# Performance work log

Measured on AMD Instinct MI355X. Metric: run time of the kernel, lower is better.

The kernel has to match this reference:

```python
import jax, jax.numpy as jnp
import numpy as np

N_HEAD = 16
N_EMBED = 2048


def setup_inputs() -> dict:
    key = jax.random.key(0)
    k1, k2, k3, k4, k5 = jax.random.split(key, 5)
    B, T, C = 4, 2048, N_EMBED
    scale = 1.0 / np.sqrt(C)
    return {
        "x": jax.random.normal(k1, (B, T, C), dtype=jnp.float32),
        "w_attn": jax.random.normal(k2, (C, 3 * C), dtype=jnp.float32) * scale,
        "b_attn": jnp.zeros((3 * C,), dtype=jnp.float32),
        "w_proj": jax.random.normal(k3, (C, C), dtype=jnp.float32) * scale,
        "b_proj": jnp.zeros((C,), dtype=jnp.float32),
    }


def reference(x, w_attn, b_attn, w_proj, b_proj):
    B, T, C = x.shape
    H = N_HEAD
    hd = C // H
    # fused QKV projection: [B,T,3C]
    qkv = jnp.einsum("btc,cd->btd", x, w_attn) + b_attn
    q, k, v = jnp.split(qkv, 3, axis=-1)
    # [B,H,T,hd]
    q = q.reshape(B, T, H, hd).transpose(0, 2, 1, 3)
    k = k.reshape(B, T, H, hd).transpose(0, 2, 1, 3)
    v = v.reshape(B, T, H, hd).transpose(0, 2, 1, 3)
    # scaled dot-product attention (no mask, no dropout at eval)
    scores = jnp.einsum("bhqd,bhkd->bhqk", q, k) / jnp.sqrt(jnp.asarray(hd, dtype=q.dtype))
    attn = jax.nn.softmax(scores, axis=-1)
    y = jnp.einsum("bhqk,bhkd->bhqd", attn, v)
    y = y.transpose(0, 2, 1, 3).reshape(B, T, C)
    return jnp.einsum("btc,cd->btd", y, w_proj) + b_proj
```

## Files before the change

kernel.cpp:

```cpp
#include <hip/hip_runtime.h>
#include <hip/hip_fp16.h>

typedef _Float16 f16;
typedef _Float16 half8 __attribute__((ext_vector_type(8)));
typedef float f32x4 __attribute__((ext_vector_type(4)));

#define NBAT 4
#define NT   2048
#define NC   2048
#define NHEAD 16
#define HD   128
#define NM   8192
#define N3C  6144
#define QK_LD 4096
#define ATT_SCALE 0.088388347648318447f

static __device__ __forceinline__ void gload16(const void* g, void* l) {
  __builtin_amdgcn_global_load_lds(
      (const __attribute__((address_space(1))) unsigned int*)g,
      (__attribute__((address_space(3))) unsigned int*)l, 16, 0, 0);
}


__global__ __launch_bounds__(256) void cvt_x_f16(const float* __restrict__ in,
                                                 f16* __restrict__ out) {
  size_t i = ((size_t)blockIdx.x * 256 + threadIdx.x) * 8;
  float4 a = *(const float4*)(in + i);
  float4 b = *(const float4*)(in + i + 4);
  half8 o;
  o[0] = (f16)a.x; o[1] = (f16)a.y; o[2] = (f16)a.z; o[3] = (f16)a.w;
  o[4] = (f16)b.x; o[5] = (f16)b.y; o[6] = (f16)b.z; o[7] = (f16)b.w;
  *(half8*)(out + i) = o;
}

__global__ __launch_bounds__(256) void cvt_tr_f16(const float* __restrict__ in,
                                                  f16* __restrict__ out,
                                                  int R, int CC) {
  __shared__ float tile[32][33];
  int cb = blockIdx.x * 32, rb = blockIdx.y * 32;
  int lx = threadIdx.x & 31, ly = threadIdx.x >> 5;
  for (int i = 0; i < 32; i += 8)
    tile[ly + i][lx] = in[(size_t)(rb + ly + i) * CC + cb + lx];
  __syncthreads();
  for (int i = 0; i < 32; i += 8)
    out[(size_t)(cb + ly + i) * R + rb + lx] = (f16)tile[lx][ly + i];
}

template <int OUTMODE>
__global__ __launch_bounds__(512, 2)
void gemm256(const f16* __restrict__ A, const f16* __restrict__ BT,
             const float* __restrict__ bias,
             f16* __restrict__ oqk, f16* __restrict__ ovT,
             float* __restrict__ of32, int N, int K, int nbn) {
  __shared__ f16 sA[4 * 8192];
  __shared__ f16 sB[4 * 8192];

  const int tid = threadIdx.x;
  const int wv = tid >> 6, lane = tid & 63;
  const int lr = lane & 15, lg = lane >> 4;
  const int wm = wv >> 2, wn = wv & 3;

  const int bid = blockIdx.x;
  const int xcd = bid & 7, li = bid >> 3;
  const int nbh = nbn >> 1;
  const int bm = (xcd & 3) * 8 + (li & 7);
  const int bn = (xcd >> 2) * nbh + (li >> 3);

  const int q0 = tid >> 3;
  const int cx = (tid & 7) ^ (q0 & 7);
  const int shi = cx >> 2, skc = cx & 3;
  const f16* aSrc = A + (size_t)(bm * 256 + q0 + 128 * shi) * K + skc * 8;
  const f16* bSrc = BT + (size_t)(bn * 256 + q0 + 128 * shi) * K + skc * 8;
  const size_t rs64 = (size_t)64 * K;
  const int ldsOff = tid * 8;

  const int NSUB = K >> 5, NKT = K >> 6;
  f32x4 acc[8][4] = {};

  auto stage = [&](int s) {
    const int sl = (s & 3) * 8192;
    const int sk = s * 32;
#pragma unroll
    for (int j = 0; j < 2; ++j) {
      gload16(aSrc + j * rs64 + sk, (void*)(sA + sl + j * 4096 + ldsOff));
      gload16(bSrc + j * rs64 + sk, (void*)(sB + sl + j * 4096 + ldsOff));
    }
  };

  stage(0); stage(1); stage(2); stage(3);

  const int ca = ((wm * 4 + lg) ^ (lr & 7)) * 8;
  const int cb = (((wn >> 1) * 4 + lg) ^ (lr & 7)) * 8;

  for (int kt = 0; kt < NKT; ++kt) {
    if (kt < NKT - 1) asm volatile("s_waitcnt vmcnt(8)" ::: "memory");
    else              asm volatile("s_waitcnt vmcnt(0)" ::: "memory");
    __builtin_amdgcn_s_barrier();
    asm volatile("" ::: "memory");

#pragma unroll
    for (int ks = 0; ks < 2; ++ks) {
      const f16* pa = sA + ((2 * kt + ks) & 3) * 8192;
      const f16* pb = sB + ((2 * kt + ks) & 3) * 8192;
      half8 a[8], b[4];
#pragma unroll
      for (int mf = 0; mf < 8; ++mf)
        a[mf] = *(const half8*)(pa + (mf * 16 + lr) * 64 + ca);
#pragma unroll
      for (int nf = 0; nf < 4; ++nf)
        b[nf] = *(const half8*)(pb + ((wn & 1) * 64 + nf * 16 + lr) * 64 + cb);
#pragma unroll
      for (int mf = 0; mf < 8; ++mf)
#pragma unroll
        for (int nf = 0; nf < 4; ++nf)
          acc[mf][nf] = __builtin_amdgcn_mfma_f32_16x16x32_f16(
              a[mf], b[nf], acc[mf][nf], 0, 0, 0);
    }
    asm volatile("" ::: "memory");
    __builtin_amdgcn_s_barrier();

    if (2 * kt + 4 < NSUB) stage(2 * kt + 4);
    if (2 * kt + 5 < NSUB) stage(2 * kt + 5);
  }

#pragma unroll
  for (int nf = 0; nf < 4; ++nf) {
    const int col = bn * 256 + wn * 64 + nf * 16 + lr;
    const float bv = bias[col];
#pragma unroll
    for (int mf = 0; mf < 8; ++mf) {
      const int row0 = bm * 256 + wm * 128 + mf * 16 + lg * 4;
      f32x4 v = acc[mf][nf];
      if (OUTMODE == 0) {
#pragma unroll
        for (int r = 0; r < 4; ++r)
          of32[(size_t)(row0 + r) * N + col] = v[r] + bv;
      } else {
        if (col < 4096) {
#pragma unroll
          for (int r = 0; r < 4; ++r)
            oqk[(size_t)(row0 + r) * QK_LD + col] = (f16)(v[r] + bv);
        } else {
          const int dfull = col - 4096;
          const int hh = dfull >> 7, dd = dfull & 127;
#pragma unroll
          for (int r = 0; r < 4; ++r) {
            const int row = row0 + r;
            const int bb = row >> 11, tt = row & 2047;
            ovT[((size_t)(bb * NHEAD + hh) * HD + dd) * NT + tt] = (f16)(v[r] + bv);
          }
        }
      }
    }
  }
}

__global__ __launch_bounds__(256, 2)
void attn_fwd(const f16* __restrict__ qk, const f16* __restrict__ vT,
              f16* __restrict__ y) {
  const int bid = blockIdx.x;
  const int sid = (bid & 7) * 128 + (bid >> 3);
  const int qt = sid & 15;
  const int bh = sid >> 4;
  const int b = bh >> 4, h = bh & 15;
  const int tid = threadIdx.x, w = tid >> 6, lane = tid & 63;
  const int lr = lane & 15, lg = lane >> 4;

  __shared__ f16 Ks[2][64 * 128];
  __shared__ f16 Vs[2][128 * 64];
  __shared__ f16 Ps[4][2][16 * 64];

  half8 qf[2][4];
  for (int s = 0; s < 2; ++s) {
    const f16* qp = qk + (size_t)(b * NT + qt * 128 + w * 32 + s * 16 + lr) * QK_LD +
                    h * HD + lg * 8;
    for (int dc = 0; dc < 4; ++dc) qf[s][dc] = *(const half8*)(qp + dc * 32);
  }

  f32x4 accy[2][8] = {};
  f32x4 lacc[2] = {};
  float mrow[2][4];
  for (int s = 0; s < 2; ++s)
    for (int r = 0; r < 4; ++r) mrow[s][r] = -1e30f;

  half8 onev;
  for (int j = 0; j < 8; ++j) onev[j] = (f16)1.0f;

  const char* kbase[4];
  const char* vbase[4];
  for (int j = 0; j < 4; ++j) {
    int idx = w * 4 + j;
    {
      int row = idx * 4 + lg;
      int swz = (lr * 16) ^ ((row & 7) << 4);
      kbase[j] = (const char*)qk +
                 ((size_t)(b * NT + row) * QK_LD + 2048 + h * HD) * 2 + swz;
    }
    {
      int d = idx * 8 + (lane >> 3);
      int cj = (lane & 7) ^ (d & 7);
      vbase[j] = (const char*)vT + ((size_t)(bh * HD + d) * NT + cj * 8) * 2;
    }
  }

  for (int j = 0; j < 4; ++j) {
    int idx = w * 4 + j;
    gload16(kbase[j], (void*)((char*)Ks[0] + idx * 1024));
    gload16(vbase[j], (void*)((char*)Vs[0] + idx * 1024));
  }

  int cur = 0;
  for (int kt = 0; kt < 32; ++kt) {
    if (kt + 1 < 32) {
      for (int j = 0; j < 4; ++j) {
        int idx = w * 4 + j;
        gload16(kbase[j] + (size_t)(kt + 1) * (64 * QK_LD * 2),
                (void*)((char*)Ks[cur ^ 1] + idx * 1024));
        gload16(vbase[j] + (size_t)(kt + 1) * 128,
                (void*)((char*)Vs[cur ^ 1] + idx * 1024));
      }
    }
    if (kt < 31) asm volatile("s_waitcnt vmcnt(8)" ::: "memory");
    else         asm volatile("s_waitcnt vmcnt(0)" ::: "memory");
    __builtin_amdgcn_s_barrier();
    asm volatile("" ::: "memory");

    f32x4 sa[2][4] = {};
    for (int nb = 0; nb < 4; ++nb) {
      int kvr = nb * 16 + lr;
      const char* kr = (const char*)Ks[cur] + kvr * 256;
      int s7 = (kvr & 7) << 4;
      for (int dc = 0; dc < 4; ++dc) {
        half8 kb = *(const half8*)(kr + ((dc * 64 + lg * 16) ^ s7));
        sa[0][nb] = __builtin_amdgcn_mfma_f32_16x16x32_f16(qf[0][dc], kb, sa[0][nb], 0, 0, 0);
        sa[1][nb] = __builtin_amdgcn_mfma_f32_16x16x32_f16(qf[1][dc], kb, sa[1][nb], 0, 0, 0);
      }
    }

    for (int s = 0; s < 2; ++s) {
      float sv[4][4];
      float pml[4] = {-1e30f, -1e30f, -1e30f, -1e30f};
      for (int nb = 0; nb < 4; ++nb)
        for (int r = 0; r < 4; ++r) {
          float x = sa[s][nb][r] * ATT_SCALE;
          sv[nb][r] = x;
          pml[r] = fmaxf(pml[r], x);
        }
      bool ok = true;
      for (int r = 0; r < 4; ++r) ok &= (pml[r] <= mrow[s][r] + 8.0f);
      if (!__all(ok)) {
        for (int r = 0; r < 4; ++r) {
          for (int off = 1; off < 16; off <<= 1)
            pml[r] = fmaxf(pml[r], __shfl_xor(pml[r], off));
          float mn = fmaxf(mrow[s][r], pml[r]);
          float al = __expf(mrow[s][r] - mn);
          mrow[s][r] = mn;
          lacc[s][r] *= al;
          for (int db = 0; db < 8; ++db) accy[s][db][r] *= al;
        }
      }
      for (int nb = 0; nb < 4; ++nb)
        for (int r = 0; r < 4; ++r) {
          float p = __expf(sv[nb][r] - mrow[s][r]);
          int prow = lg * 4 + r;
          int chunk = (nb * 2 + (lr >> 3)) ^ (prow & 7);
          Ps[w][s][prow * 64 + chunk * 8 + (lr & 7)] = (f16)p;
        }
    }

    half8 pa[2][2];
    for (int s = 0; s < 2; ++s)
      for (int kc = 0; kc < 2; ++kc) {
        int chunk = (kc * 4 + lg) ^ (lr & 7);
        pa[s][kc] = *(const half8*)(&Ps[w][s][lr * 64 + chunk * 8]);
      }
    for (int s = 0; s < 2; ++s)
      for (int kc = 0; kc < 2; ++kc)
        lacc[s] = __builtin_amdgcn_mfma_f32_16x16x32_f16(pa[s][kc], onev, lacc[s], 0, 0, 0);

    for (int db = 0; db < 8; ++db) {
      int d = db * 16 + lr;
      const char* vr = (const char*)Vs[cur] + d * 128;
      int d7 = d & 7;
      for (int kc = 0; kc < 2; ++kc) {
        half8 vb = *(const half8*)(vr + (((kc * 4 + lg) ^ d7) * 16));
        accy[0][db] = __builtin_amdgcn_mfma_f32_16x16x32_f16(pa[0][kc], vb, accy[0][db], 0, 0, 0);
        accy[1][db] = __builtin_amdgcn_mfma_f32_16x16x32_f16(pa[1][kc], vb, accy[1][db], 0, 0, 0);
      }
    }

    asm volatile("" ::: "memory");
    __builtin_amdgcn_s_barrier();
    cur ^= 1;
  }

  for (int s = 0; s < 2; ++s) {
    f32x4 inv;
    for (int r = 0; r < 4; ++r) inv[r] = 1.0f / lacc[s][r];
    f16* yp = y + (size_t)(b * NT + qt * 128 + w * 32 + s * 16 + lg * 4) * NC +
              h * HD + lr;
    for (int db = 0; db < 8; ++db)
      for (int r = 0; r < 4; ++r)
        yp[(size_t)r * NC + db * 16] = (f16)(accy[s][db][r] * inv[r]);
  }
}

extern "C" void kernel_launch(void* const* d_in, const int* in_sizes, int n_in,
                              void* d_out, int out_size, void* d_ws, size_t ws_size,
                              hipStream_t stream) {
  (void)in_sizes; (void)n_in; (void)out_size; (void)ws_size;
  const float* x      = (const float*)d_in[0];
  const float* w_attn = (const float*)d_in[1];
  const float* b_attn = (const float*)d_in[2];
  const float* w_proj = (const float*)d_in[3];
  const float* b_proj = (const float*)d_in[4];
  float* out = (float*)d_out;

  char* p = (char*)d_ws;
  f16* xh  = (f16*)p; p += (size_t)NM * NC * 2;
  f16* waT = (f16*)p; p += (size_t)N3C * NC * 2;
  f16* wpT = (f16*)p; p += (size_t)NC * NC * 2;
  f16* qkb = (f16*)p; p += (size_t)NM * QK_LD * 2;
  f16* vT  = (f16*)p; p += (size_t)NBAT * NHEAD * HD * NT * 2;
  f16* yh  = (f16*)p; p += (size_t)NM * NC * 2;

  cvt_x_f16<<<8192, 256, 0, stream>>>(x, xh);
  cvt_tr_f16<<<dim3(192, 64), 256, 0, stream>>>(w_attn, waT, NC, N3C);
  cvt_tr_f16<<<dim3(64, 64), 256, 0, stream>>>(w_proj, wpT, NC, NC);
  gemm256<1><<<768, 512, 0, stream>>>(xh, waT, b_attn, qkb, vT, nullptr,
                                      N3C, NC, 24);
  attn_fwd<<<1024, 256, 0, stream>>>(qkb, vT, yh);
  gemm256<0><<<256, 512, 0, stream>>>(yh, wpT, b_proj, nullptr, nullptr,
                                      out, NC, NC, 8);
}
```

Measured before the change: 553.1 us.

## Restructure GEMM main loop into fine-grained 8-phase pipeline with interleaved loads

Rewrites the 256x256 GEMM mainloop so each iteration is split into eight phases. Each phase loads a small A fragment from LDS, issues one half-tile global-to-LDS prefetch for a future K step, synchronises, then runs a burst of MFMAs at raised wave priority. Block-to-tile mapping changes to a simple XCD-strided linear order, and the LDS layout becomes 64-wide K tiles split into two M/N halves. The aim is to overlap memory traffic with matrix math more evenly, at the cost of many more barriers per K step.

```diff
diff --git a/kernel.cpp b/kernel.cpp
--- a/kernel.cpp
+++ b/kernel.cpp
@@ -60,67 +60,96 @@
   const int lr = lane & 15, lg = lane >> 4;
   const int wm = wv >> 2, wn = wv & 3;
 
-  const int bid = blockIdx.x;
-  const int xcd = bid & 7, li = bid >> 3;
-  const int nbh = nbn >> 1;
-  const int bm = (xcd & 3) * 8 + (li & 7);
-  const int bn = (xcd >> 2) * nbh + (li >> 3);
+  const int q8 = gridDim.x >> 3;
+  const int sid = ((int)blockIdx.x & 7) * q8 + ((int)blockIdx.x >> 3);
+  const int bm = sid / nbn, bn = sid % nbn;
 
   const int q0 = tid >> 3;
   const int cx = (tid & 7) ^ (q0 & 7);
-  const int shi = cx >> 2, skc = cx & 3;
-  const f16* aSrc = A + (size_t)(bm * 256 + q0 + 128 * shi) * K + skc * 8;
-  const f16* bSrc = BT + (size_t)(bn * 256 + q0 + 128 * shi) * K + skc * 8;
-  const size_t rs64 = (size_t)64 * K;
-  const int ldsOff = tid * 8;
-
-  const int NSUB = K >> 5, NKT = K >> 6;
+  const f16* aSrc = A + (size_t)(bm * 256 + q0) * K + cx * 8;
+  const f16* bSrc = BT + (size_t)(bn * 256 + q0) * K + cx * 8;
+  const size_t rs64 = (size_t)64 * K, rs128 = (size_t)128 * K;
+
+  const int NKT = K >> 6, NIT = NKT >> 1;
   f32x4 acc[8][4] = {};
 
-  auto stage = [&](int s) {
-    const int sl = (s & 3) * 8192;
-    const int sk = s * 32;
-#pragma unroll
-    for (int j = 0; j < 2; ++j) {
-      gload16(aSrc + j * rs64 + sk, (void*)(sA + sl + j * 4096 + ldsOff));
-      gload16(bSrc + j * rs64 + sk, (void*)(sB + sl + j * 4096 + ldsOff));
-    }
+  auto stgA = [&](int t, int h, int bu) {
+    const f16* s = aSrc + (size_t)h * rs128 + t * 64;
+    f16* d = sA + (bu * 2 + h) * 8192 + tid * 8;
+    gload16(s, d);
+    gload16(s + rs64, d + 4096);
   };
-
-  stage(0); stage(1); stage(2); stage(3);
-
-  const int ca = ((wm * 4 + lg) ^ (lr & 7)) * 8;
-  const int cb = (((wn >> 1) * 4 + lg) ^ (lr & 7)) * 8;
-
-  for (int kt = 0; kt < NKT; ++kt) {
-    if (kt < NKT - 1) asm volatile("s_waitcnt vmcnt(8)" ::: "memory");
-    else              asm volatile("s_waitcnt vmcnt(0)" ::: "memory");
-    __builtin_amdgcn_s_barrier();
-    asm volatile("" ::: "memory");
-
-#pragma unroll
-    for (int ks = 0; ks < 2; ++ks) {
-      const f16* pa = sA + ((2 * kt + ks) & 3) * 8192;
-      const f16* pb = sB + ((2 * kt + ks) & 3) * 8192;
-      half8 a[8], b[4];
-#pragma unroll
-      for (int mf = 0; mf < 8; ++mf)
-        a[mf] = *(const half8*)(pa + (mf * 16 + lr) * 64 + ca);
-#pragma unroll
-      for (int nf = 0; nf < 4; ++nf)
-        b[nf] = *(const half8*)(pb + ((wn & 1) * 64 + nf * 16 + lr) * 64 + cb);
-#pragma unroll
-      for (int mf = 0; mf < 8; ++mf)
+  auto stgB = [&](int t, int h, int bu) {
+    const f16* s = bSrc + (size_t)h * rs128 + t * 64;
+    f16* d = sB + (bu * 2 + h) * 8192 + tid * 8;
+    gload16(s, d);
+    gload16(s + rs64, d + 4096);
+  };
+
+  stgA(0, 0, 0); stgA(0, 1, 0);
+  stgB(0, 0, 0); stgB(0, 1, 0);
+  stgB(1, 0, 1); stgB(1, 1, 1);
+  asm volatile("s_waitcnt vmcnt(4)" ::: "memory");
+  __builtin_amdgcn_s_barrier();
+  asm volatile("" ::: "memory");
+
+  const int xcs[2] = {((0 * 4 + lg) ^ (lr & 7)) * 8, ((1 * 4 + lg) ^ (lr & 7)) * 8};
+
+  for (int it = 0; it < NIT; ++it) {
+    const int u = 2 * it, v = u + 1;
+    const bool notlast = (it < NIT - 1);
+    half8 bfrag[4][2];
+#pragma unroll
+    for (int p = 0; p < 8; ++p) {
+      const int buf = (p < 4) ? 0 : 1;
+      const f16* bA = sA + (buf * 2 + wm) * 8192;
+      const f16* bB = sB + (buf * 2 + (wn >> 1)) * 8192;
+      const int mf0 = (p & 3) * 2;
+      if ((p & 3) == 0) {
 #pragma unroll
         for (int nf = 0; nf < 4; ++nf)
-          acc[mf][nf] = __builtin_amdgcn_mfma_f32_16x16x32_f16(
-              a[mf], b[nf], acc[mf][nf], 0, 0, 0);
-    }
-    asm volatile("" ::: "memory");
-    __builtin_amdgcn_s_barrier();
-
-    if (2 * kt + 4 < NSUB) stage(2 * kt + 4);
-    if (2 * kt + 5 < NSUB) stage(2 * kt + 5);
+#pragma unroll
+          for (int ks = 0; ks < 2; ++ks)
+            bfrag[nf][ks] = *(const half8*)(
+                bB + ((wn & 1) * 64 + nf * 16 + lr) * 64 + xcs[ks]);
+      }
+      half8 afrag[2][2];
+#pragma unroll
+      for (int m2 = 0; m2 < 2; ++m2)
+#pragma unroll
+        for (int ks = 0; ks < 2; ++ks)
+          afrag[m2][ks] = *(const half8*)(
+              bA + ((mf0 + m2) * 16 + lr) * 64 + xcs[ks]);
+      switch (p) {
+        case 0: stgA(v, 0, 1); break;
+        case 1: stgA(v, 1, 1); break;
+        case 2: if (notlast) stgB(u + 2, 0, 0); break;
+        case 3: if (notlast) stgB(u + 2, 1, 0); break;
+        case 4: if (notlast) stgA(u + 2, 0, 0); break;
+        case 5: if (notlast) stgA(u + 2, 1, 0); break;
+        case 6: if (notlast) stgB(v + 2, 0, 1); break;
+        case 7: if (notlast) stgB(v + 2, 1, 1); break;
+      }
+      if ((p & 3) == 3) {
+        if (notlast) asm volatile("s_waitcnt vmcnt(4)" ::: "memory");
+        else         asm volatile("s_waitcnt vmcnt(0)" ::: "memory");
+      }
+      asm volatile("" ::: "memory");
+      __builtin_amdgcn_s_barrier();
+      asm volatile("" ::: "memory");
+      __builtin_amdgcn_s_setprio(1);
+#pragma unroll
+      for (int m2 = 0; m2 < 2; ++m2)
+#pragma unroll
+        for (int nf = 0; nf < 4; ++nf)
+#pragma unroll
+          for (int ks = 0; ks < 2; ++ks)
+            acc[mf0 + m2][nf] = __builtin_amdgcn_mfma_f32_16x16x32_f16(
+                afrag[m2][ks], bfrag[nf][ks], acc[mf0 + m2][nf], 0, 0, 0);
+      __builtin_amdgcn_s_setprio(0);
+      asm volatile("" ::: "memory");
+      __builtin_amdgcn_s_barrier();
+    }
   }
 
 #pragma unroll
```

Measured after the change: 483.7 us. 12.5% less time.
